# Optimization experiments

Hardware: AMD Instinct MI355X
Metric: run time of the kernel (lower is better)

## Reference

```python
import jax, jax.numpy as jnp
import numpy as np

B, C, CQK, H, W = 4, 256, 64, 64, 64


def setup_inputs() -> dict:
    key = jax.random.key(0)
    ks = jax.random.split(key, 8)
    scale = 1.0 / np.sqrt(C)
    features = jax.random.normal(ks[0], (B, C, H, W), dtype=jnp.float32)
    Wq = jax.random.normal(ks[1], (CQK, C), dtype=jnp.float32) * scale
    bq = jax.random.normal(ks[2], (CQK,), dtype=jnp.float32) * 0.01
    Wk = jax.random.normal(ks[3], (CQK, C), dtype=jnp.float32) * scale
    bk = jax.random.normal(ks[4], (CQK,), dtype=jnp.float32) * 0.01
    Wv = jax.random.normal(ks[5], (C, C), dtype=jnp.float32) * scale
    bv = jax.random.normal(ks[6], (C,), dtype=jnp.float32) * 0.01
    # nn.Parameter(torch.zeros(1)) in the original; use a nonzero value so the
    # attention path contributes to the output (and gradients) during testing.
    weight = jax.random.normal(ks[7], (1,), dtype=jnp.float32) * 0.5
    return {"features": features, "Wq": Wq, "bq": bq, "Wk": Wk, "bk": bk,
            "Wv": Wv, "bv": bv, "weight": weight}


def reference(features, Wq, bq, Wk, bk, Wv, bv, weight):
    b, c, h, w = features.shape
    x = features.reshape(b, c, h * w)                       # [B, C, N]
    # 1x1 convs == channel-mixing matmuls
    q = jnp.einsum('oc,bcn->bon', Wq, x) + bq[None, :, None]  # [B, CQK, N]
    k = jnp.einsum('oc,bcn->bon', Wk, x) + bk[None, :, None]  # [B, CQK, N]
    v = jnp.einsum('oc,bcn->bon', Wv, x) + bv[None, :, None]  # [B, C, N]
    # energy[b,i,j] = <q[:, i], k[:, j]>; softmax over keys j
    energy = jnp.einsum('bci,bcj->bij', q, k)                 # [B, N, N]
    attention = jax.nn.softmax(energy, axis=-1)
    # out[b,c,i] = sum_j v[b,c,j] * attention[b,i,j]
    out = jnp.einsum('bcj,bij->bci', v, attention)            # [B, C, N]
    return (weight[0] * out + x).reshape(b, c, h, w)
```

## Files before the change

kernel.cpp:

```cpp
#include <hip/hip_runtime.h>
#include <hip/hip_bf16.h>

constexpr int BB  = 4;
constexpr int CC  = 256;
constexpr int CQ  = 64;
constexpr int NN  = 4096;
constexpr int KS  = 4;
constexpr int QTR = 128;
constexpr int KVB = 32;

typedef __attribute__((ext_vector_type(8))) short bf16x8;
typedef __attribute__((ext_vector_type(4))) float f32x4;

__device__ __forceinline__ short f2bf(float f) {
    unsigned u = __float_as_uint(f);
    unsigned r = u + 0x7fffu + ((u >> 16) & 1u);
    return (short)(r >> 16);
}

__device__ __forceinline__ short f2bf_fast(float f) {
    __bf16 h = (__bf16)f;
    return *reinterpret_cast<short*>(&h);
}

__device__ __forceinline__ void gload16(const void* gsrc, void* ldst) {
    __builtin_amdgcn_global_load_lds(
        (const __attribute__((address_space(1))) unsigned int*)gsrc,
        (__attribute__((address_space(3))) unsigned int*)ldst, 16, 0, 0);
}

__global__ __launch_bounds__(256, 3) void proj_kernel(
        const float* __restrict__ x,
        const float* __restrict__ Wq, const float* __restrict__ bq,
        const float* __restrict__ Wk, const float* __restrict__ bk,
        const float* __restrict__ Wv, const float* __restrict__ bv,
        short* __restrict__ Qt, short* __restrict__ Kt,
        short* __restrict__ Vm) {
    const int id  = blockIdx.x;
    const int xcd = id & 7, sub = id >> 3;
    const int b   = xcd >> 1;
    const int og  = sub >> 4;
    const int ntl = ((xcd & 1) << 4) + (sub & 15);
    const int n0  = ntl * 128;

    const int t    = threadIdx.x;
    const int wv   = t >> 6;
    const int lane = t & 63;
    const int l15  = lane & 15;
    const int g    = lane >> 4;

    __shared__ __align__(16) short Wl[64 * 256];
    __shared__ __align__(16) short Xl[2][128 * 40];

    const float* Wsrc; const float* bsrc; float scale;
    if (og == 0)      { Wsrc = Wq;                  bsrc = bq;               scale = 1.4426950408889634f; }
    else if (og == 1) { Wsrc = Wk;                  bsrc = bk;               scale = 1.0f; }
    else              { Wsrc = Wv + (og - 2) * 64 * 256; bsrc = bv + (og - 2) * 64; scale = 1.0f; }

    {
        const int oc = t >> 2, kb = (t & 3) * 64;
        const float* wr = Wsrc + oc * 256 + kb;
#pragma unroll
        for (int cc = 0; cc < 8; ++cc) {
            bf16x8 wchunk;
#pragma unroll
            for (int e = 0; e < 8; ++e) wchunk[e] = f2bf_fast(wr[cc * 8 + e] * scale);
            const int c = (kb >> 3) + cc;
            char* dst = (char*)Wl + oc * 512 + ((c * 16) ^ ((oc & 7) << 4));
            *(bf16x8*)dst = wchunk;
        }
    }

    const int xn   = t & 127;
    const int half = t >> 7;
    const float* xb = x + (size_t)b * CC * NN + n0 + xn;
    const int swn  = ((xn & 3) ^ ((xn >> 3) & 3));

    auto stageX = [&](int kc, int buf) {
        const float* xr = xb + (size_t)(kc * 32 + half * 16) * NN;
        float v[16];
#pragma unroll
        for (int kk = 0; kk < 16; ++kk) v[kk] = xr[(size_t)kk * NN];
#pragma unroll
        for (int cc = 0; cc < 2; ++cc) {
            bf16x8 pk;
#pragma unroll
            for (int e = 0; e < 8; ++e) pk[e] = f2bf_fast(v[cc * 8 + e]);
            const int c = half * 2 + cc;
            char* dst = (char*)&Xl[buf][0] + xn * 80 + ((c ^ swn) << 4);
            *(bf16x8*)dst = pk;
        }
    };

    f32x4 acc[8];
#pragma unroll
    for (int nf = 0; nf < 8; ++nf) acc[nf] = (f32x4){0.f, 0.f, 0.f, 0.f};

    stageX(0, 0);

    const int ocr = wv * 16 + l15;
    for (int kc = 0; kc < 8; ++kc) {
        __syncthreads();
        if (kc < 7) stageX(kc + 1, (kc + 1) & 1);

        const char* wsrcl = (const char*)Wl + ocr * 512
                          + (((kc * 4 + g) * 16) ^ ((ocr & 7) << 4));
        bf16x8 af = *(const bf16x8*)wsrcl;

        const char* xbase = (const char*)&Xl[kc & 1][0];
#pragma unroll
        for (int nf = 0; nf < 8; ++nf) {
            const int n = nf * 16 + l15;
            const int swr = ((n & 3) ^ ((n >> 3) & 3));
            bf16x8 bf = *(const bf16x8*)(xbase + n * 80 + ((g ^ swr) << 4));
            acc[nf] = __builtin_amdgcn_mfma_f32_16x16x32_bf16(af, bf, acc[nf], 0, 0, 0);
        }
    }

    float bias4[4];
#pragma unroll
    for (int r = 0; r < 4; ++r) bias4[r] = bsrc[wv * 16 + g * 4 + r] * scale;

    if (og < 2) {
        short* base = (og == 0 ? Qt : Kt) + (size_t)b * NN * 64;
#pragma unroll
        for (int nf = 0; nf < 8; ++nf) {
            const int n = n0 + nf * 16 + l15;
            short4 pk;
            pk.x = f2bf_fast(acc[nf][0] + bias4[0]);
            pk.y = f2bf_fast(acc[nf][1] + bias4[1]);
            pk.z = f2bf_fast(acc[nf][2] + bias4[2]);
            pk.w = f2bf_fast(acc[nf][3] + bias4[3]);
            *(short4*)(base + (size_t)n * 64 + wv * 16 + g * 4) = pk;
        }
    } else {
        short* vb = Vm + (size_t)b * CC * NN;
        const int c0 = (og - 2) * 64 + wv * 16 + g * 4;
#pragma unroll
        for (int nf = 0; nf < 8; ++nf) {
            const int n = n0 + nf * 16 + l15;
#pragma unroll
            for (int r = 0; r < 4; ++r)
                vb[(size_t)(c0 + r) * NN + n] = f2bf_fast(acc[nf][r] + bias4[r]);
        }
    }
}

__global__ __launch_bounds__(256, 2) void flash_kernel(
        const short* __restrict__ Qt, const short* __restrict__ Kt,
        const short* __restrict__ Vm,
        short* __restrict__ Opart, float* __restrict__ Lp) {
    const int id  = blockIdx.x;
    const int xcd = id & 7, sub = id >> 3;
    const int b   = xcd >> 1;
    const int qt  = sub & 31;
    const int ks  = ((xcd & 1) << 1) | (sub >> 5);

    const int wave = threadIdx.x >> 6;
    const int lane = threadIdx.x & 63;
    const int l15  = lane & 15;
    const int g    = lane >> 4;

    __shared__ short Kl[2][KVB * 64];
    __shared__ short Vl[2][CC * KVB];

    const short* Qb = Qt + (size_t)b * NN * 64;
    const short* Kb = Kt + (size_t)b * NN * 64;
    const short* Vb = Vm + (size_t)b * CC * NN;

    const int qbase = qt * QTR + wave * 32;

    bf16x8 qf[2][2];
#pragma unroll
    for (int rf = 0; rf < 2; ++rf)
#pragma unroll
        for (int kk = 0; kk < 2; ++kk)
            qf[rf][kk] = *(const bf16x8*)(Qb + (size_t)(qbase + rf * 16 + l15) * 64
                                          + kk * 32 + g * 8);

    float lsum_p[2] = {0.0f, 0.0f};

    f32x4 oacc[2][16];
#pragma unroll
    for (int rf = 0; rf < 2; ++rf)
#pragma unroll
        for (int ch = 0; ch < 16; ++ch) oacc[rf][ch] = (f32x4){0.f, 0.f, 0.f, 0.f};

    const int k_off0 = l15 * 128 + ((g * 16)      ^ ((l15 & 7) << 4));
    const int k_off1 = l15 * 128 + ((64 + g * 16) ^ ((l15 & 7) << 4));
    const int v_off  = l15 * 64  + ((g * 16) ^ (((l15 >> 1) & 3) << 4));

    const int vrow_off = lane >> 2;
    const int vscol    = (((lane & 3) ^ ((lane >> 3) & 3)) << 4);
    const int krow_off = lane >> 3;
    const int kscol    = (((lane & 7) ^ (lane >> 3)) << 4);

    auto stage = [&](int buf, int kbase) {
#pragma unroll
        for (int i = 0; i < 5; ++i) {
            const int s = wave * 5 + i;
            if (s < 16) {
                const int row = s * 16 + vrow_off;
                const char* src = (const char*)(Vb + (size_t)row * NN + kbase) + vscol;
                gload16(src, (char*)&Vl[buf][0] + s * 1024);
            } else {
                const int ss = s - 16;
                const int j  = ss * 8 + krow_off;
                const int sj = (((j & 15) >> 2) << 3) + ((j >> 4) << 2) + (j & 3);
                const char* src = (const char*)(Kb + (size_t)(kbase + sj) * 64) + kscol;
                gload16(src, (char*)&Kl[buf][0] + ss * 1024);
            }
        }
    };

    const int kt0 = ks * (NN / KS);
    stage(0, kt0);

    for (int it = 0; it < NN / KS / KVB; ++it) {
        const int cur = it & 1;
        __syncthreads();
        if (it < NN / KS / KVB - 1) stage(cur ^ 1, kt0 + (it + 1) * KVB);

        const char* klb = (const char*)&Kl[cur][0];
        const char* vlb = (const char*)&Vl[cur][0];

        __builtin_amdgcn_s_setprio(1);
        f32x4 s2[2][2];
#pragma unroll
        for (int jt = 0; jt < 2; ++jt) {
            bf16x8 kf0 = *(const bf16x8*)(klb + jt * 2048 + k_off0);
            bf16x8 kf1 = *(const bf16x8*)(klb + jt * 2048 + k_off1);
#pragma unroll
            for (int rf = 0; rf < 2; ++rf) {
                f32x4 a = (f32x4){0.f, 0.f, 0.f, 0.f};
                a = __builtin_amdgcn_mfma_f32_16x16x32_bf16(kf0, qf[rf][0], a, 0, 0, 0);
                a = __builtin_amdgcn_mfma_f32_16x16x32_bf16(kf1, qf[rf][1], a, 0, 0, 0);
                s2[rf][jt] = a;
            }
        }
        __builtin_amdgcn_s_setprio(0);

        bf16x8 pf[2];
#pragma unroll
        for (int rf = 0; rf < 2; ++rf) {
#pragma unroll
            for (int jt = 0; jt < 2; ++jt)
#pragma unroll
                for (int r = 0; r < 4; ++r) {
                    float p = exp2f(s2[rf][jt][r]);
                    lsum_p[rf] += p;
                    pf[rf][jt * 4 + r] = f2bf_fast(p);
                }
        }

        __builtin_amdgcn_s_setprio(1);
#pragma unroll
        for (int ch = 0; ch < 16; ++ch) {
            bf16x8 vf = *(const bf16x8*)(vlb + ch * 1024 + v_off);
#pragma unroll
            for (int rf = 0; rf < 2; ++rf)
                oacc[rf][ch] = __builtin_amdgcn_mfma_f32_16x16x32_bf16(pf[rf], vf,
                                                                       oacc[rf][ch], 0, 0, 0);
        }
        __builtin_amdgcn_s_setprio(0);
    }

    const int pt = (b * 32 + qt) * KS + ks;
    short* Op = Opart + (size_t)pt * QTR * 256;
#pragma unroll
    for (int rf = 0; rf < 2; ++rf)
#pragma unroll
        for (int ch = 0; ch < 16; ++ch)
#pragma unroll
            for (int r = 0; r < 4; ++r)
                Op[(size_t)(wave * 32 + rf * 16 + g * 4 + r) * 256 + ch * 16 + l15] =
                    f2bf_fast(oacc[rf][ch][r]);
#pragma unroll
    for (int rf = 0; rf < 2; ++rf) {
        float v = lsum_p[rf];
        v += __shfl_xor(v, 16);
        v += __shfl_xor(v, 32);
        if (lane < 16)
            Lp[(size_t)pt * QTR + wave * 32 + rf * 16 + lane] = v;
    }
}

__global__ __launch_bounds__(256) void combine_kernel(
        const short* __restrict__ Opart, const float* __restrict__ Lp,
        const float* __restrict__ x, const float* __restrict__ weightp,
        float* __restrict__ out) {
    const int b     = blockIdx.x;
    const int rowg0 = blockIdx.y * 32;
    const int qt    = rowg0 >> 7;
    const int rbase = rowg0 & 127;
    const int t     = threadIdx.x;

    __shared__ float oc[32][257];
    __shared__ float linv[32];

    const int pt0 = (b * 32 + qt) * KS;

    if (t < 32) {
        const size_t mb = (size_t)pt0 * QTR + rbase + t;
        float L = 0.f;
#pragma unroll
        for (int s = 0; s < KS; ++s) L += Lp[mb + (size_t)s * QTR];
        linv[t] = 1.0f / L;
    }
    __syncthreads();

    const size_t ob = (size_t)pt0 * QTR * 256 + (size_t)rbase * 256;
    const int cp = t & 127;
    const int rh = t >> 7;
#pragma unroll 4
    for (int rr = 0; rr < 16; ++rr) {
        const int row = rh * 16 + rr;
        float a0 = 0.f, a1 = 0.f;
#pragma unroll
        for (int s = 0; s < KS; ++s) {
            unsigned u = *(const unsigned*)
                &Opart[ob + (size_t)s * QTR * 256 + row * 256 + cp * 2];
            a0 += __uint_as_float(u << 16);
            a1 += __uint_as_float(u & 0xffff0000u);
        }
        const float li = linv[row];
        oc[row][cp * 2]     = a0 * li;
        oc[row][cp * 2 + 1] = a1 * li;
    }
    __syncthreads();

    const float wgt = weightp[0];
    const int row = t & 31, cg = t >> 5;
    const float* xb = x + (size_t)b * CC * NN + rowg0 + row;
    float* op = out + (size_t)b * CC * NN + rowg0 + row;
#pragma unroll 4
    for (int c = cg; c < 256; c += 8) {
        op[(size_t)c * NN] = wgt * oc[row][c] + xb[(size_t)c * NN];
    }
}

extern "C" void kernel_launch(void* const* d_in, const int* in_sizes, int n_in,
                              void* d_out, int out_size, void* d_ws, size_t ws_size,
                              hipStream_t stream) {
    const float* feat = (const float*)d_in[0];
    const float* Wq   = (const float*)d_in[1];
    const float* bq   = (const float*)d_in[2];
    const float* Wk   = (const float*)d_in[3];
    const float* bk   = (const float*)d_in[4];
    const float* Wv   = (const float*)d_in[5];
    const float* bv   = (const float*)d_in[6];
    const float* wgt  = (const float*)d_in[7];
    float* out = (float*)d_out;

    short* Qt = (short*)d_ws;
    short* Kt = Qt + (size_t)BB * NN * CQ;
    short* Vm = Kt + (size_t)BB * NN * CQ;
    short* Opart = Vm + (size_t)BB * CC * NN;
    float* Lp = (float*)(Opart + (size_t)BB * 32 * KS * QTR * 256);

    proj_kernel<<<dim3(768), 256, 0, stream>>>(
        feat, Wq, bq, Wk, bk, Wv, bv, Qt, Kt, Vm);

    flash_kernel<<<dim3(BB * 32 * KS), 256, 0, stream>>>(
        Qt, Kt, Vm, Opart, Lp);

    combine_kernel<<<dim3(BB, NN / 32), 256, 0, stream>>>(
        Opart, Lp, feat, wgt, out);
}
```

Measured before the change: 86.87 us.

## Enlarge flash tiles to 256 queries and 64 keys with 8-wave 2D split

The flash kernel now runs 512-thread blocks covering 256 query rows, with KV tiles of 64 keys. The eight waves are arranged as 4 row groups by 2 channel halves, so each wave holds 64 query rows against 128 value channels. Each K/V tile loaded into LDS is therefore reused by twice as many queries, and exp/softmax work is fused directly after the QK MFMAs. The grid shrinks to 256 blocks, which may underfill the GPU. Per-wave register pressure rises, and QK^T plus exp is computed redundantly by both channel-half waves.

Result: slower. 112.0 us (+28.9%).

```diff
diff --git a/kernel.cpp b/kernel.cpp
--- a/kernel.cpp
+++ b/kernel.cpp
@@ -6,8 +6,8 @@
 constexpr int CQ  = 64;
 constexpr int NN  = 4096;
 constexpr int KS  = 4;
-constexpr int QTR = 128;
-constexpr int KVB = 32;
+constexpr int QTR = 256;
+constexpr int KVB = 64;
 
 typedef __attribute__((ext_vector_type(8))) short bf16x8;
 typedef __attribute__((ext_vector_type(4))) float f32x4;
@@ -146,17 +146,19 @@
     }
 }
 
-__global__ __launch_bounds__(256, 2) void flash_kernel(
+__global__ __launch_bounds__(512, 2) void flash_kernel(
         const short* __restrict__ Qt, const short* __restrict__ Kt,
         const short* __restrict__ Vm,
         short* __restrict__ Opart, float* __restrict__ Lp) {
     const int id  = blockIdx.x;
     const int xcd = id & 7, sub = id >> 3;
     const int b   = xcd >> 1;
-    const int qt  = sub & 31;
-    const int ks  = ((xcd & 1) << 1) | (sub >> 5);
+    const int qt  = sub & 15;
+    const int ks  = ((xcd & 1) << 1) | (sub >> 4);
 
     const int wave = threadIdx.x >> 6;
+    const int rg   = wave >> 1;
+    const int cg   = wave & 1;
     const int lane = threadIdx.x & 63;
     const int l15  = lane & 15;
     const int g    = lane >> 4;
@@ -168,46 +170,45 @@
     const short* Kb = Kt + (size_t)b * NN * 64;
     const short* Vb = Vm + (size_t)b * CC * NN;
 
-    const int qbase = qt * QTR + wave * 32;
-
-    bf16x8 qf[2][2];
-#pragma unroll
-    for (int rf = 0; rf < 2; ++rf)
+    const int qbase = qt * QTR + rg * 64;
+
+    bf16x8 qf[4][2];
+#pragma unroll
+    for (int rf = 0; rf < 4; ++rf)
 #pragma unroll
         for (int kk = 0; kk < 2; ++kk)
             qf[rf][kk] = *(const bf16x8*)(Qb + (size_t)(qbase + rf * 16 + l15) * 64
                                           + kk * 32 + g * 8);
 
-    float lsum_p[2] = {0.0f, 0.0f};
-
-    f32x4 oacc[2][16];
-#pragma unroll
-    for (int rf = 0; rf < 2; ++rf)
-#pragma unroll
-        for (int ch = 0; ch < 16; ++ch) oacc[rf][ch] = (f32x4){0.f, 0.f, 0.f, 0.f};
+    float lsum_p[4] = {0.f, 0.f, 0.f, 0.f};
+
+    f32x4 oacc[4][8];
+#pragma unroll
+    for (int rf = 0; rf < 4; ++rf)
+#pragma unroll
+        for (int chf = 0; chf < 8; ++chf) oacc[rf][chf] = (f32x4){0.f, 0.f, 0.f, 0.f};
 
     const int k_off0 = l15 * 128 + ((g * 16)      ^ ((l15 & 7) << 4));
     const int k_off1 = l15 * 128 + ((64 + g * 16) ^ ((l15 & 7) << 4));
-    const int v_off  = l15 * 64  + ((g * 16) ^ (((l15 >> 1) & 3) << 4));
-
-    const int vrow_off = lane >> 2;
-    const int vscol    = (((lane & 3) ^ ((lane >> 3) & 3)) << 4);
-    const int krow_off = lane >> 3;
-    const int kscol    = (((lane & 7) ^ (lane >> 3)) << 4);
+
+    const int r8   = lane >> 3;
+    const int scol = (((lane & 7) ^ r8) << 4);
 
     auto stage = [&](int buf, int kbase) {
 #pragma unroll
         for (int i = 0; i < 5; ++i) {
             const int s = wave * 5 + i;
-            if (s < 16) {
-                const int row = s * 16 + vrow_off;
-                const char* src = (const char*)(Vb + (size_t)row * NN + kbase) + vscol;
+            if (s < 32) {
+                const int row = s * 8 + r8;
+                const char* src = (const char*)(Vb + (size_t)row * NN + kbase) + scol;
                 gload16(src, (char*)&Vl[buf][0] + s * 1024);
             } else {
-                const int ss = s - 16;
-                const int j  = ss * 8 + krow_off;
-                const int sj = (((j & 15) >> 2) << 3) + ((j >> 4) << 2) + (j & 3);
-                const char* src = (const char*)(Kb + (size_t)(kbase + sj) * 64) + kscol;
+                const int ss   = s - 32;
+                const int slot = ss * 8 + r8;
+                const int h    = slot >> 5, j = slot & 31;
+                const int sj   = (((j & 15) >> 2) << 3) + ((j >> 4) << 2) + (j & 3);
+                const char* src = (const char*)(Kb + (size_t)(kbase + h * 32 + sj) * 64)
+                                + scol;
                 gload16(src, (char*)&Kl[buf][0] + ss * 1024);
             }
         }
@@ -222,66 +223,63 @@
         if (it < NN / KS / KVB - 1) stage(cur ^ 1, kt0 + (it + 1) * KVB);
 
         const char* klb = (const char*)&Kl[cur][0];
-        const char* vlb = (const char*)&Vl[cur][0];
-
-        __builtin_amdgcn_s_setprio(1);
-        f32x4 s2[2][2];
-#pragma unroll
-        for (int jt = 0; jt < 2; ++jt) {
+        const char* vlb = (const char*)&Vl[cur][0] + cg * 16384;
+
+        bf16x8 pf[4][2];
+#pragma unroll
+        for (int jt = 0; jt < 4; ++jt) {
             bf16x8 kf0 = *(const bf16x8*)(klb + jt * 2048 + k_off0);
             bf16x8 kf1 = *(const bf16x8*)(klb + jt * 2048 + k_off1);
-#pragma unroll
-            for (int rf = 0; rf < 2; ++rf) {
+            const int h = jt >> 1, e0 = (jt & 1) * 4;
+#pragma unroll
+            for (int rf = 0; rf < 4; ++rf) {
                 f32x4 a = (f32x4){0.f, 0.f, 0.f, 0.f};
                 a = __builtin_amdgcn_mfma_f32_16x16x32_bf16(kf0, qf[rf][0], a, 0, 0, 0);
                 a = __builtin_amdgcn_mfma_f32_16x16x32_bf16(kf1, qf[rf][1], a, 0, 0, 0);
-                s2[rf][jt] = a;
+#pragma unroll
+                for (int r = 0; r < 4; ++r) {
+                    float p = exp2f(a[r]);
+                    lsum_p[rf] += p;
+                    pf[rf][h][e0 + r] = f2bf_fast(p);
+                }
             }
         }
+
+        __builtin_amdgcn_s_setprio(1);
+#pragma unroll
+        for (int chf = 0; chf < 8; ++chf) {
+            bf16x8 vf0 = *(const bf16x8*)(vlb + chf * 2048 + k_off0);
+            bf16x8 vf1 = *(const bf16x8*)(vlb + chf * 2048 + k_off1);
+#pragma unroll
+            for (int rf = 0; rf < 4; ++rf) {
+                oacc[rf][chf] = __builtin_amdgcn_mfma_f32_16x16x32_bf16(pf[rf][0], vf0,
+                                                                        oacc[rf][chf], 0, 0, 0);
+                oacc[rf][chf] = __builtin_amdgcn_mfma_f32_16x16x32_bf16(pf[rf][1], vf1,
+                                                                        oacc[rf][chf], 0, 0, 0);
+            }
+        }
         __builtin_amdgcn_s_setprio(0);
-
-        bf16x8 pf[2];
-#pragma unroll
-        for (int rf = 0; rf < 2; ++rf) {
-#pragma unroll
-            for (int jt = 0; jt < 2; ++jt)
-#pragma unroll
-                for (int r = 0; r < 4; ++r) {
-                    float p = exp2f(s2[rf][jt][r]);
-                    lsum_p[rf] += p;
-                    pf[rf][jt * 4 + r] = f2bf_fast(p);
-                }
-        }
-
-        __builtin_amdgcn_s_setprio(1);
-#pragma unroll
-        for (int ch = 0; ch < 16; ++ch) {
-            bf16x8 vf = *(const bf16x8*)(vlb + ch * 1024 + v_off);
-#pragma unroll
-            for (int rf = 0; rf < 2; ++rf)
-                oacc[rf][ch] = __builtin_amdgcn_mfma_f32_16x16x32_bf16(pf[rf], vf,
-                                                                       oacc[rf][ch], 0, 0, 0);
-        }
-        __builtin_amdgcn_s_setprio(0);
-    }
-
-    const int pt = (b * 32 + qt) * KS + ks;
+    }
+
+    const int pt = (b * 16 + qt) * KS + ks;
     short* Op = Opart + (size_t)pt * QTR * 256;
 #pragma unroll
-    for (int rf = 0; rf < 2; ++rf)
-#pragma unroll
-        for (int ch = 0; ch < 16; ++ch)
+    for (int rf = 0; rf < 4; ++rf)
+#pragma unroll
+        for (int chf = 0; chf < 8; ++chf)
 #pragma unroll
             for (int r = 0; r < 4; ++r)
-                Op[(size_t)(wave * 32 + rf * 16 + g * 4 + r) * 256 + ch * 16 + l15] =
-                    f2bf_fast(oacc[rf][ch][r]);
-#pragma unroll
-    for (int rf = 0; rf < 2; ++rf) {
-        float v = lsum_p[rf];
-        v += __shfl_xor(v, 16);
-        v += __shfl_xor(v, 32);
-        if (lane < 16)
-            Lp[(size_t)pt * QTR + wave * 32 + rf * 16 + lane] = v;
+                Op[(size_t)(rg * 64 + rf * 16 + g * 4 + r) * 256
+                   + cg * 128 + chf * 16 + l15] = f2bf_fast(oacc[rf][chf][r]);
+    if (cg == 0) {
+#pragma unroll
+        for (int rf = 0; rf < 4; ++rf) {
+            float v = lsum_p[rf];
+            v += __shfl_xor(v, 16);
+            v += __shfl_xor(v, 32);
+            if (lane < 16)
+                Lp[(size_t)pt * QTR + rg * 64 + rf * 16 + lane] = v;
+        }
     }
 }
 
@@ -291,14 +289,14 @@
         float* __restrict__ out) {
     const int b     = blockIdx.x;
     const int rowg0 = blockIdx.y * 32;
-    const int qt    = rowg0 >> 7;
-    const int rbase = rowg0 & 127;
+    const int qt    = rowg0 >> 8;
+    const int rbase = rowg0 & 255;
     const int t     = threadIdx.x;
 
     __shared__ float oc[32][257];
     __shared__ float linv[32];
 
-    const int pt0 = (b * 32 + qt) * KS;
+    const int pt0 = (b * 16 + qt) * KS;
 
     if (t < 32) {
         const size_t mb = (size_t)pt0 * QTR + rbase + t;
@@ -356,12 +354,12 @@
     short* Kt = Qt + (size_t)BB * NN * CQ;
     short* Vm = Kt + (size_t)BB * NN * CQ;
     short* Opart = Vm + (size_t)BB * CC * NN;
-    float* Lp = (float*)(Opart + (size_t)BB * 32 * KS * QTR * 256);
+    float* Lp = (float*)(Opart + (size_t)BB * 16 * KS * QTR * 256);
 
     proj_kernel<<<dim3(768), 256, 0, stream>>>(
         feat, Wq, bq, Wk, bk, Wv, bv, Qt, Kt, Vm);
 
-    flash_kernel<<<dim3(BB * 32 * KS), 256, 0, stream>>>(
+    flash_kernel<<<dim3(BB * 16 * KS), 512, 0, stream>>>(
         Qt, Kt, Vm, Opart, Lp);
 
     combine_kernel<<<dim3(BB, NN / 32), 256, 0, stream>>>(
```
